# Performance work log

Hardware: AMD Instinct MI355X
Metric: run time of the kernel (lower is better)

Reference implementation:

```python
import jax, jax.numpy as jnp
import numpy as np

DT = 0.001  # euler step size (module default dt)
T = 2000    # num_timesteps
N_IN = 8192
N_OUT = 4096


def setup_inputs() -> dict:
    key = jax.random.key(0)
    k_x, k_w = jax.random.split(key)
    x = jax.random.normal(k_x, (T, N_IN), dtype=jnp.float32)
    # module initializes weight.data.uniform_(-0.1, 0.1)
    weight = jax.random.uniform(k_w, (N_OUT, N_IN), dtype=jnp.float32, minval=-0.1, maxval=0.1)
    ones = jnp.ones((N_OUT,), dtype=jnp.float32)
    # default_lif_parameters broadcast to per-neuron vectors (constant_lif_parameters)
    return {
        "x": x,
        "weight": weight,
        "v_th": ones * 75.0,
        "v_rest": ones * 50.0,
        "v_reset": ones * 30.0,
        "t_ref": ones * 0.001,
        "tau": ones * 2.0,
    }


def reference(x, weight, v_th, v_rest, v_reset, t_ref, tau):
    # lif_input[t] = x[t] @ weight.T  -> [T, N_OUT]
    lif_input = x @ weight.T

    def step(carry, inp):
        v, refrac = carry
        # leak toward v_rest
        v = v - DT * tau * (v - v_rest)
        # integrate input only when not refractory
        v = v + jnp.where(refrac == 0, inp, jnp.zeros_like(inp))
        # count down refractory period
        refrac = jnp.where(refrac > 0, refrac - DT, jnp.zeros_like(refrac))
        # heavyside spike
        spike = (v - v_th >= 0).astype(v.dtype)
        sb = spike > 0
        # reset: refractory period and membrane potential
        refrac = jnp.where(sb, t_ref, refrac)
        v = jnp.where(sb, v_reset, v)
        return (v, refrac), spike

    v0 = v_rest.astype(x.dtype)               # v[0] = v_rest
    refrac0 = jnp.zeros_like(v0)
    # torch loop runs i = 1 .. T-1 consuming lif_input[i]
    _, spikes = jax.lax.scan(step, (v0, refrac0), lif_input[1:])
    s0 = jnp.zeros((1, spikes.shape[1]), dtype=spikes.dtype)  # s[0] stays zero
    return jnp.concatenate([s0, spikes], axis=0)  # [T, N_OUT]
```

## Files before the change

### kernel.cpp

```cpp
#include <hip/hip_runtime.h>
#include <hip/hip_bf16.h>


#define T_STEPS 2000
#define NIN_K   8192
#define NOUT_N  4096
#define MPAD    2048

typedef __attribute__((ext_vector_type(8))) _Float16 half8;
typedef __attribute__((ext_vector_type(4))) float f32x4;

#define GLL16(g, l)                                                              \
    __builtin_amdgcn_global_load_lds(                                            \
        (const __attribute__((address_space(1))) void*)(g),                      \
        (__attribute__((address_space(3))) void*)(l), 16, 0, 0)

__global__ __launch_bounds__(256) void split_f32(const float* __restrict__ src,
                                                 _Float16* __restrict__ hi,
                                                 _Float16* __restrict__ lo,
                                                 size_t n_valid) {
    const size_t i8 = (size_t)(blockIdx.x * 256u + threadIdx.x) * 8;
    float vv[8];
    if (i8 < n_valid) {
        float4 v0 = *(const float4*)(src + i8);
        float4 v1 = *(const float4*)(src + i8 + 4);
        vv[0] = v0.x; vv[1] = v0.y; vv[2] = v0.z; vv[3] = v0.w;
        vv[4] = v1.x; vv[5] = v1.y; vv[6] = v1.z; vv[7] = v1.w;
    } else {
#pragma unroll
        for (int j = 0; j < 8; ++j) vv[j] = 0.f;
    }
    half8 h8, l8;
#pragma unroll
    for (int j = 0; j < 8; ++j) {
        _Float16 h = (_Float16)vv[j];
        float r = __fsub_rn(vv[j], (float)h);
        h8[j] = h;
        l8[j] = (_Float16)(r * 4096.0f);
    }
    *(half8*)(hi + i8) = h8;
    *(half8*)(lo + i8) = l8;
}

__global__ __launch_bounds__(256, 2) void gemm_f16x2(const _Float16* __restrict__ A0,
                                                     const _Float16* __restrict__ A1,
                                                     const _Float16* __restrict__ B0,
                                                     const _Float16* __restrict__ B1,
                                                     float* __restrict__ C) {
    __shared__ _Float16 lds[4][128 * 32];

    const int tid  = threadIdx.x;
    const int wave = tid >> 6;
    const int lane = tid & 63;
    const int bm = blockIdx.y * 128;
    const int bn = blockIdx.x * 128;
    const int wm = (wave >> 1) * 64;
    const int wn = (wave & 1) * 64;

    const int srow  = tid >> 2;
    const int skoff = (tid & 3) * 8;

    f32x4 acc0[4][4], acc1[4][4];
#pragma unroll
    for (int i = 0; i < 4; ++i)
#pragma unroll
        for (int j = 0; j < 4; ++j) {
            acc0[i][j] = (f32x4){0.f, 0.f, 0.f, 0.f};
            acc1[i][j] = (f32x4){0.f, 0.f, 0.f, 0.f};
        }

    const int quad = lane >> 4;
    const int l16  = lane & 15;

    for (int k0 = 0; k0 < NIN_K; k0 += 32) {
        __syncthreads();
#pragma unroll
        for (int c = 0; c < 2; ++c) {
            const size_t ga = (size_t)(bm + c * 64 + srow) * NIN_K + k0 + skoff;
            const size_t gb = (size_t)(bn + c * 64 + srow) * NIN_K + k0 + skoff;
            const int ldst = (c * 64 + wave * 16) * 32;
            GLL16(A0 + ga, &lds[0][ldst]);
            GLL16(A1 + ga, &lds[1][ldst]);
            GLL16(B0 + gb, &lds[2][ldst]);
            GLL16(B1 + gb, &lds[3][ldst]);
        }
        __syncthreads();

        half8 b0f[4], b1f[4];
#pragma unroll
        for (int j = 0; j < 4; ++j) {
            const int off = (wn + j * 16 + l16) * 32 + quad * 8;
            b0f[j] = *(const half8*)&lds[2][off];
            b1f[j] = *(const half8*)&lds[3][off];
        }
#pragma unroll
        for (int i = 0; i < 4; ++i) {
            const int off = (wm + i * 16 + l16) * 32 + quad * 8;
            const half8 a0f = *(const half8*)&lds[0][off];
            const half8 a1f = *(const half8*)&lds[1][off];
#pragma unroll
            for (int j = 0; j < 4; ++j) {
                acc0[i][j] = __builtin_amdgcn_mfma_f32_16x16x32_f16(a0f, b0f[j], acc0[i][j], 0, 0, 0);
                acc1[i][j] = __builtin_amdgcn_mfma_f32_16x16x32_f16(a0f, b1f[j], acc1[i][j], 0, 0, 0);
                acc1[i][j] = __builtin_amdgcn_mfma_f32_16x16x32_f16(a1f, b0f[j], acc1[i][j], 0, 0, 0);
            }
        }
    }

    const float s = 1.0f / 4096.0f;
#pragma unroll
    for (int i = 0; i < 4; ++i)
#pragma unroll
        for (int j = 0; j < 4; ++j) {
            const int m = bm + wm + i * 16 + quad * 4;
            const int n = bn + wn + j * 16 + l16;
            float* cp = C + (size_t)m * NOUT_N + n;
#pragma unroll
            for (int r = 0; r < 4; ++r)
                cp[(size_t)r * NOUT_N] = __fmaf_rn(acc1[i][j][r], s, acc0[i][j][r]);
        }
}

#define BM 64
#define BN 64
#define BK 16
#define PAD 4
__global__ __launch_bounds__(256) void gemm_bt(const float* __restrict__ A,
                                               const float* __restrict__ B,
                                               float* __restrict__ C,
                                               int M, int N, int K) {
    __shared__ float As[BK][BM + PAD];
    __shared__ float Bs[BK][BN + PAD];
    const int bm = blockIdx.y * BM, bn = blockIdx.x * BN;
    const int tid = threadIdx.x;
    const int tx = tid & 15, ty = tid >> 4;
    const int lrow = tid >> 2, lk = (tid & 3) * 4;
    float acc[4][4];
#pragma unroll
    for (int i = 0; i < 4; ++i)
#pragma unroll
        for (int j = 0; j < 4; ++j) acc[i][j] = 0.0f;
    for (int k0 = 0; k0 < K; k0 += BK) {
        const int am = bm + lrow;
        float4 av = (am < M) ? *(const float4*)(A + (size_t)am * K + k0 + lk)
                             : make_float4(0.f, 0.f, 0.f, 0.f);
        As[lk + 0][lrow] = av.x; As[lk + 1][lrow] = av.y;
        As[lk + 2][lrow] = av.z; As[lk + 3][lrow] = av.w;
        float4 bv = *(const float4*)(B + (size_t)(bn + lrow) * K + k0 + lk);
        Bs[lk + 0][lrow] = bv.x; Bs[lk + 1][lrow] = bv.y;
        Bs[lk + 2][lrow] = bv.z; Bs[lk + 3][lrow] = bv.w;
        __syncthreads();
#pragma unroll
        for (int k = 0; k < BK; ++k) {
            float a[4], b[4];
#pragma unroll
            for (int i = 0; i < 4; ++i) a[i] = As[k][ty * 4 + i];
#pragma unroll
            for (int j = 0; j < 4; ++j) b[j] = Bs[k][tx * 4 + j];
#pragma unroll
            for (int i = 0; i < 4; ++i)
#pragma unroll
                for (int j = 0; j < 4; ++j) acc[i][j] += a[i] * b[j];
        }
        __syncthreads();
    }
#pragma unroll
    for (int i = 0; i < 4; ++i) {
        const int m = bm + ty * 4 + i;
        if (m < M) {
            float* cp = C + (size_t)m * N + bn + tx * 4;
#pragma unroll
            for (int j = 0; j < 4; ++j) cp[j] = acc[i][j];
        }
    }
}

#define SCAN_D 32
__global__ __launch_bounds__(64) void lif_scan(const float* __restrict__ inp,
                                               const float* __restrict__ v_th_p,
                                               const float* __restrict__ v_rest_p,
                                               const float* __restrict__ v_reset_p,
                                               const float* __restrict__ t_ref_p,
                                               const float* __restrict__ tau_p,
                                               float* __restrict__ out,
                                               int T, int N) {
    const int j = blockIdx.x * 64 + threadIdx.x;
    if (j >= N) return;
    const float vth = v_th_p[j], vrest = v_rest_p[j], vres = v_reset_p[j];
    const float tref = t_ref_p[j];
    const float c = __fmul_rn(0.001f, tau_p[j]);
    float v = vrest, refrac = 0.0f;
    out[j] = 0.0f;

    float pf[SCAN_D];
#pragma unroll
    for (int d = 0; d < SCAN_D; ++d) pf[d] = inp[(size_t)(1 + d) * N + j];

    int base = 1;
    for (; base + SCAN_D <= T; base += SCAN_D) {
#pragma unroll
        for (int d = 0; d < SCAN_D; ++d) {
            const float in = pf[d];
            int tf = base + d + SCAN_D;
            tf = (tf < T) ? tf : (T - 1);
            pf[d] = inp[(size_t)tf * N + j];
            const float dd = __fmul_rn(c, __fsub_rn(v, vrest));
            v = __fsub_rn(v, dd);
            v = (refrac == 0.0f) ? __fadd_rn(v, in) : v;
            refrac = (refrac > 0.0f) ? (refrac - 0.001f) : 0.0f;
            const bool s = (__fsub_rn(v, vth) >= 0.0f);
            out[(size_t)(base + d) * N + j] = s ? 1.0f : 0.0f;
            refrac = s ? tref : refrac;
            v = s ? vres : v;
        }
    }
#pragma unroll
    for (int d = 0; d < SCAN_D; ++d) {
        const int t = base + d;
        if (t < T) {
            const float in = pf[d];
            const float dd = __fmul_rn(c, __fsub_rn(v, vrest));
            v = __fsub_rn(v, dd);
            v = (refrac == 0.0f) ? __fadd_rn(v, in) : v;
            refrac = (refrac > 0.0f) ? (refrac - 0.001f) : 0.0f;
            const bool s = (__fsub_rn(v, vth) >= 0.0f);
            out[(size_t)t * N + j] = s ? 1.0f : 0.0f;
            refrac = s ? tref : refrac;
            v = s ? vres : v;
        }
    }
}

extern "C" void kernel_launch(void* const* d_in, const int* in_sizes, int n_in,
                              void* d_out, int out_size, void* d_ws, size_t ws_size,
                              hipStream_t stream) {
    const float* x       = (const float*)d_in[0];
    const float* w       = (const float*)d_in[1];
    const float* v_th    = (const float*)d_in[2];
    const float* v_rest  = (const float*)d_in[3];
    const float* v_reset = (const float*)d_in[4];
    const float* t_ref   = (const float*)d_in[5];
    const float* tau     = (const float*)d_in[6];
    float* out = (float*)d_out;

    const size_t LIF_B = (size_t)MPAD * NOUT_N * 4;
    const size_t XS_B  = (size_t)MPAD * NIN_K * 2;
    const size_t WS_B  = (size_t)NOUT_N * NIN_K * 2;
    const size_t NEED  = LIF_B + 2 * XS_B + 2 * WS_B;

    char* ws = (char*)d_ws;
    float* lif = (float*)ws;

    if (ws_size >= NEED) {
        _Float16* x0 = (_Float16*)(ws + LIF_B);
        _Float16* x1 = (_Float16*)(ws + LIF_B + XS_B);
        _Float16* w0 = (_Float16*)(ws + LIF_B + 2 * XS_B);
        _Float16* w1 = (_Float16*)(ws + LIF_B + 2 * XS_B + WS_B);

        const size_t nx = (size_t)MPAD * NIN_K;
        split_f32<<<nx / 8 / 256, 256, 0, stream>>>(x, x0, x1,
                                                    (size_t)T_STEPS * NIN_K);
        const size_t nw = (size_t)NOUT_N * NIN_K;
        split_f32<<<nw / 8 / 256, 256, 0, stream>>>(w, w0, w1, nw);

        dim3 g(NOUT_N / 128, MPAD / 128);
        gemm_f16x2<<<g, 256, 0, stream>>>(x0, x1, w0, w1, lif);
    } else {
        dim3 g(NOUT_N / BN, (T_STEPS + BM - 1) / BM);
        gemm_bt<<<g, 256, 0, stream>>>(x, w, lif, T_STEPS, NOUT_N, NIN_K);
    }

    lif_scan<<<NOUT_N / 64, 64, 0, stream>>>(lif, v_th, v_rest, v_reset, t_ref, tau,
                                             out, T_STEPS, NOUT_N);
}
```

Baseline: 791.5 us.

## Double GEMM K-tile to 64 with XOR-swizzled LDS and simplify LIF scan

The GEMM now stages 64-wide K tiles instead of 32, which halves the number of barrier pairs per K sweep. It uses an XOR swizzle on the LDS column chunks to avoid bank conflicts in the fragment reads. LDS use doubles to 64 KB per block, which may reduce occupancy below the 2-blocks hint. The LIF scan is specialized to fixed T with a 16-deep prefetch that reads into the padded rows without clamping, and a zero_rows kernel pads the fallback path's buffer to keep those reads safe.

```diff
diff --git a/kernel.cpp b/kernel.cpp
--- a/kernel.cpp
+++ b/kernel.cpp
@@ -47,7 +47,7 @@
                                                      const _Float16* __restrict__ B0,
                                                      const _Float16* __restrict__ B1,
                                                      float* __restrict__ C) {
-    __shared__ _Float16 lds[4][128 * 32];
+    __shared__ _Float16 lds[4][128 * 64];
 
     const int tid  = threadIdx.x;
     const int wave = tid >> 6;
@@ -57,8 +57,8 @@
     const int wm = (wave >> 1) * 64;
     const int wn = (wave & 1) * 64;
 
-    const int srow  = tid >> 2;
-    const int skoff = (tid & 3) * 8;
+    const int srow = tid >> 3;
+    const int skswz = ((tid & 7) ^ (srow & 7)) * 8;
 
     f32x4 acc0[4][4], acc1[4][4];
 #pragma unroll
@@ -72,37 +72,42 @@
     const int quad = lane >> 4;
     const int l16  = lane & 15;
 
-    for (int k0 = 0; k0 < NIN_K; k0 += 32) {
-        __syncthreads();
-#pragma unroll
-        for (int c = 0; c < 2; ++c) {
-            const size_t ga = (size_t)(bm + c * 64 + srow) * NIN_K + k0 + skoff;
-            const size_t gb = (size_t)(bn + c * 64 + srow) * NIN_K + k0 + skoff;
-            const int ldst = (c * 64 + wave * 16) * 32;
-            GLL16(A0 + ga, &lds[0][ldst]);
-            GLL16(A1 + ga, &lds[1][ldst]);
-            GLL16(B0 + gb, &lds[2][ldst]);
-            GLL16(B1 + gb, &lds[3][ldst]);
-        }
-        __syncthreads();
-
-        half8 b0f[4], b1f[4];
-#pragma unroll
-        for (int j = 0; j < 4; ++j) {
-            const int off = (wn + j * 16 + l16) * 32 + quad * 8;
-            b0f[j] = *(const half8*)&lds[2][off];
-            b1f[j] = *(const half8*)&lds[3][off];
-        }
-#pragma unroll
-        for (int i = 0; i < 4; ++i) {
-            const int off = (wm + i * 16 + l16) * 32 + quad * 8;
-            const half8 a0f = *(const half8*)&lds[0][off];
-            const half8 a1f = *(const half8*)&lds[1][off];
+    for (int k0 = 0; k0 < NIN_K; k0 += 64) {
+        __syncthreads();
+#pragma unroll
+        for (int c = 0; c < 4; ++c) {
+            const size_t ga = (size_t)(bm + c * 32 + srow) * NIN_K + k0 + skswz;
+            const size_t gb = (size_t)(bn + c * 32 + srow) * NIN_K + k0 + skswz;
+            const int base = (c * 32 + wave * 8) * 64;
+            GLL16(A0 + ga, &lds[0][base]);
+            GLL16(A1 + ga, &lds[1][base]);
+            GLL16(B0 + gb, &lds[2][base]);
+            GLL16(B1 + gb, &lds[3][base]);
+        }
+        __syncthreads();
+
+#pragma unroll
+        for (int ks = 0; ks < 2; ++ks) {
+            half8 b0f[4], b1f[4];
 #pragma unroll
             for (int j = 0; j < 4; ++j) {
-                acc0[i][j] = __builtin_amdgcn_mfma_f32_16x16x32_f16(a0f, b0f[j], acc0[i][j], 0, 0, 0);
-                acc1[i][j] = __builtin_amdgcn_mfma_f32_16x16x32_f16(a0f, b1f[j], acc1[i][j], 0, 0, 0);
-                acc1[i][j] = __builtin_amdgcn_mfma_f32_16x16x32_f16(a1f, b0f[j], acc1[i][j], 0, 0, 0);
+                const int row = wn + j * 16 + l16;
+                const int off = row * 64 + ((ks * 4 + quad) ^ (row & 7)) * 8;
+                b0f[j] = *(const half8*)&lds[2][off];
+                b1f[j] = *(const half8*)&lds[3][off];
+            }
+#pragma unroll
+            for (int i = 0; i < 4; ++i) {
+                const int row = wm + i * 16 + l16;
+                const int off = row * 64 + ((ks * 4 + quad) ^ (row & 7)) * 8;
+                const half8 a0f = *(const half8*)&lds[0][off];
+                const half8 a1f = *(const half8*)&lds[1][off];
+#pragma unroll
+                for (int j = 0; j < 4; ++j) {
+                    acc0[i][j] = __builtin_amdgcn_mfma_f32_16x16x32_f16(a0f, b0f[j], acc0[i][j], 0, 0, 0);
+                    acc1[i][j] = __builtin_amdgcn_mfma_f32_16x16x32_f16(a0f, b1f[j], acc1[i][j], 0, 0, 0);
+                    acc1[i][j] = __builtin_amdgcn_mfma_f32_16x16x32_f16(a1f, b0f[j], acc1[i][j], 0, 0, 0);
+                }
             }
         }
     }
@@ -175,50 +180,37 @@
     }
 }
 
-#define SCAN_D 32
+__global__ void zero_rows(float* __restrict__ p, size_t n) {
+    const size_t i = (size_t)blockIdx.x * 256 + threadIdx.x;
+    if (i < n) p[i] = 0.0f;
+}
+
 __global__ __launch_bounds__(64) void lif_scan(const float* __restrict__ inp,
                                                const float* __restrict__ v_th_p,
                                                const float* __restrict__ v_rest_p,
                                                const float* __restrict__ v_reset_p,
                                                const float* __restrict__ t_ref_p,
                                                const float* __restrict__ tau_p,
-                                               float* __restrict__ out,
-                                               int T, int N) {
+                                               float* __restrict__ out) {
     const int j = blockIdx.x * 64 + threadIdx.x;
-    if (j >= N) return;
+    const int N = NOUT_N;
     const float vth = v_th_p[j], vrest = v_rest_p[j], vres = v_reset_p[j];
     const float tref = t_ref_p[j];
     const float c = __fmul_rn(0.001f, tau_p[j]);
     float v = vrest, refrac = 0.0f;
     out[j] = 0.0f;
 
-    float pf[SCAN_D];
-#pragma unroll
-    for (int d = 0; d < SCAN_D; ++d) pf[d] = inp[(size_t)(1 + d) * N + j];
-
-    int base = 1;
-    for (; base + SCAN_D <= T; base += SCAN_D) {
-#pragma unroll
-        for (int d = 0; d < SCAN_D; ++d) {
+    float pf[16];
+#pragma unroll
+    for (int d = 0; d < 16; ++d) pf[d] = inp[(size_t)(1 + d) * N + j];
+
+    for (int g = 0; g < 124; ++g) {
+        const int tbase = 1 + g * 16;
+#pragma unroll
+        for (int d = 0; d < 16; ++d) {
+            const int t = tbase + d;
             const float in = pf[d];
-            int tf = base + d + SCAN_D;
-            tf = (tf < T) ? tf : (T - 1);
-            pf[d] = inp[(size_t)tf * N + j];
-            const float dd = __fmul_rn(c, __fsub_rn(v, vrest));
-            v = __fsub_rn(v, dd);
-            v = (refrac == 0.0f) ? __fadd_rn(v, in) : v;
-            refrac = (refrac > 0.0f) ? (refrac - 0.001f) : 0.0f;
-            const bool s = (__fsub_rn(v, vth) >= 0.0f);
-            out[(size_t)(base + d) * N + j] = s ? 1.0f : 0.0f;
-            refrac = s ? tref : refrac;
-            v = s ? vres : v;
-        }
-    }
-#pragma unroll
-    for (int d = 0; d < SCAN_D; ++d) {
-        const int t = base + d;
-        if (t < T) {
-            const float in = pf[d];
+            pf[d] = inp[(size_t)(t + 16) * N + j];
             const float dd = __fmul_rn(c, __fsub_rn(v, vrest));
             v = __fsub_rn(v, dd);
             v = (refrac == 0.0f) ? __fadd_rn(v, in) : v;
@@ -228,6 +220,19 @@
             refrac = s ? tref : refrac;
             v = s ? vres : v;
         }
+    }
+#pragma unroll
+    for (int e = 0; e < 15; ++e) {
+        const int t = 1985 + e;
+        const float in = pf[e];
+        const float dd = __fmul_rn(c, __fsub_rn(v, vrest));
+        v = __fsub_rn(v, dd);
+        v = (refrac == 0.0f) ? __fadd_rn(v, in) : v;
+        refrac = (refrac > 0.0f) ? (refrac - 0.001f) : 0.0f;
+        const bool s = (__fsub_rn(v, vth) >= 0.0f);
+        out[(size_t)t * N + j] = s ? 1.0f : 0.0f;
+        refrac = s ? tref : refrac;
+        v = s ? vres : v;
     }
 }
 
@@ -268,8 +273,9 @@
     } else {
         dim3 g(NOUT_N / BN, (T_STEPS + BM - 1) / BM);
         gemm_bt<<<g, 256, 0, stream>>>(x, w, lif, T_STEPS, NOUT_N, NIN_K);
-    }
-
-    lif_scan<<<NOUT_N / 64, 64, 0, stream>>>(lif, v_th, v_rest, v_reset, t_ref, tau,
-                                             out, T_STEPS, NOUT_N);
-}
+        const size_t padn = (size_t)(MPAD - T_STEPS) * NOUT_N;
+        zero_rows<<<(padn + 255) / 256, 256, 0, stream>>>(lif + (size_t)T_STEPS * NOUT_N, padn);
+    }
+
+    lif_scan<<<NOUT_N / 64, 64, 0, stream>>>(lif, v_th, v_rest, v_reset, t_ref, tau, out);
+}
```

Result: faster. 721.4 us (-8.9%).
